# Kernel optimization log

Measured on AMD Instinct MI355X. Metric: run time of the kernel, lower is better.

## Reference

```python
import jax, jax.numpy as jnp
import numpy as np

M = 4  # mixture size of the AttentionStem value embedding

def unfold_windows(a, kh, kw, Hout, Wout):
    # a: [..., Hp, Wp] -> [..., Hout, Wout, kh, kw] (stride-1 sliding windows, cropped)
    rows = []
    for i in range(kh):
        cols = [a[..., i:i + Hout, j:j + Wout] for j in range(kw)]
        rows.append(jnp.stack(cols, axis=-1))
    return jnp.stack(rows, axis=-2)

def attention_stem(x, qw, kw_, vw, emb_a, emb_b, emb_mix, kh, kw, pad):
    # x: [B,Cin,H,W]; qw/kw_: [Cin,Co]; vw: [M,Cin,Co]; emb_a:[Co,kh]; emb_b:[Co,kw]; emb_mix:[M,Co]
    B, Cin, H, W = x.shape
    pl, pr, pt, pb = pad  # F.pad order (left,right,top,bottom)
    xp = jnp.pad(x, ((0, 0), (0, 0), (pt, pb), (pl, pr)))
    Hp, Wp = xp.shape[2], xp.shape[3]
    Hout = min(Hp - kh + 1, H)
    Wout = min(Wp - kw + 1, W)
    q = jnp.einsum('bchw,co->bohw', x[:, :, :Hout, :Wout], qw)       # 1x1 conv query
    k = jnp.einsum('bchw,co->bohw', xp, kw_)                          # 1x1 conv key on padded
    v = jnp.einsum('bchw,mco->mbohw', xp, vw)                         # m 1x1 conv values
    k_win = unfold_windows(k, kh, kw, Hout, Wout)                     # [B,Co,Ho,Wo,kh,kw]
    v_win = unfold_windows(v, kh, kw, Hout, Wout)                     # [M,B,Co,Ho,Wo,kh,kw]
    # mixture relative-position embedding, softmax over mixtures per (kh,kw) offset
    la = emb_mix @ emb_a                                              # [M,kh]
    lb = emb_mix @ emb_b                                              # [M,kw]
    emb = jax.nn.softmax(la[:, :, None] + lb[:, None, :], axis=0)     # [M,kh,kw]
    v_agg = jnp.einsum('mkl,mbohwkl->bohwkl', emb, v_win)             # [B,Co,Ho,Wo,kh,kw]
    K = kh * kw
    scores = jnp.einsum('bohw,bohwkl->bhwkl', q, k_win).reshape(B, Hout, Wout, K)
    attn = jax.nn.softmax(scores, axis=-1).reshape(B, Hout, Wout, kh, kw)
    out = jnp.einsum('bhwkl,bohwkl->bohw', attn, v_agg)               # [B,Co,Ho,Wo]
    return out

def bn_relu(x, g, b):
    # training-mode BatchNorm2d + ReLU
    mu = x.mean(axis=(0, 2, 3), keepdims=True)
    var = x.var(axis=(0, 2, 3), keepdims=True)
    y = (x - mu) * jax.lax.rsqrt(var + 1e-5) * g[None, :, None, None] + b[None, :, None, None]
    return jax.nn.relu(y)

def _params(key):
    ks = jax.random.split(key, 18)
    def w(k, shape):
        return jax.random.normal(k, shape, dtype=jnp.float32) * 0.1
    cfg = [(1, 64, 1, 5), (64, 128, 2, 5), (128, 16, 2, 5)]
    p = {}
    i = 0
    for s, (ci, co, kh, kw) in enumerate(cfg):
        p[f'p{s}_q'] = w(ks[i], (ci, co)); i += 1
        p[f'p{s}_k'] = w(ks[i], (ci, co)); i += 1
        p[f'p{s}_v'] = w(ks[i], (M, ci, co)); i += 1
        p[f'p{s}_ea'] = w(ks[i], (co, kh)); i += 1
        p[f'p{s}_eb'] = w(ks[i], (co, kw)); i += 1
        p[f'p{s}_em'] = w(ks[i], (M, co)); i += 1
        p[f'p{s}_g'] = jnp.ones((co,), jnp.float32)
        p[f'p{s}_b'] = jnp.zeros((co,), jnp.float32)
    return p

def setup_inputs() -> dict:
    key = jax.random.key(0)
    kx, kp = jax.random.split(key)
    inp = {'x': jax.random.normal(kx, (2, 1, 8, 3000), dtype=jnp.float32)}
    inp.update(_params(kp))
    return inp

def reference(x,
              p0_q, p0_k, p0_v, p0_ea, p0_eb, p0_em, p0_g, p0_b,
              p1_q, p1_k, p1_v, p1_ea, p1_eb, p1_em, p1_g, p1_b,
              p2_q, p2_k, p2_v, p2_ea, p2_eb, p2_em, p2_g, p2_b):
    h = attention_stem(x, p0_q, p0_k, p0_v, p0_ea, p0_eb, p0_em, 1, 5, (2, 2, 0, 0))
    h = bn_relu(h, p0_g, p0_b)[:, :, ::2, ::2]                        # MaxPool2d(1,2) == stride-2 subsample
    h = attention_stem(h, p1_q, p1_k, p1_v, p1_ea, p1_eb, p1_em, 2, 5, (2, 2, 1, 1))
    h = bn_relu(h, p1_g, p1_b)[:, :, ::2, ::2]
    h = attention_stem(h, p2_q, p2_k, p2_v, p2_ea, p2_eb, p2_em, 2, 5, (2, 2, 0, 0))
    h = bn_relu(h, p2_g, p2_b)
    B, C, H, W = h.shape
    nW = W // 56                                                       # AvgPool2d((1,56))
    return h[:, :, :, :nW * 56].reshape(B, C, H, nW, 56).mean(-1)
```

## Files before the change

kernel.cpp:

```cpp
#include <hip/hip_runtime.h>
#include <math.h>


#define TPB 256

__global__ void prep0_kernel(const float* __restrict__ ea,
                             const float* __restrict__ eb,
                             const float* __restrict__ em,
                             const float* __restrict__ qw,
                             const float* __restrict__ kw_,
                             const float* __restrict__ vw,
                             float* __restrict__ par) {
    const int M4 = 4, Co = 64, kw = 5;
    __shared__ float la[4];
    __shared__ float lb[20];
    __shared__ float embs[20];
    int tid = threadIdx.x;
    if (tid < 64) {
        float p = qw[tid] * kw_[tid];
#pragma unroll
        for (int d = 1; d < 64; d <<= 1) p += __shfl_xor(p, d, 64);
        if (tid == 0) par[0] = p;
    }
    if (tid >= 64 && tid < 64 + M4) {
        int m = tid - 64;
        float s = 0.f;
        for (int o = 0; o < Co; ++o) s += em[m * Co + o] * ea[o];
        la[m] = s;
    }
    if (tid >= 128 && tid < 128 + M4 * kw) {
        int r = tid - 128;
        int m = r / kw, l = r % kw;
        float s = 0.f;
        for (int o = 0; o < Co; ++o) s += em[m * Co + o] * eb[o * kw + l];
        lb[m * kw + l] = s;
    }
    __syncthreads();
    if (tid < 5) {
        float lg[4];
        float mx = -1e30f;
        for (int m = 0; m < M4; ++m) {
            lg[m] = la[m] + lb[m * kw + tid];
            mx = fmaxf(mx, lg[m]);
        }
        float sum = 0.f;
        for (int m = 0; m < M4; ++m) { lg[m] = expf(lg[m] - mx); sum += lg[m]; }
        float inv = 1.f / sum;
        for (int m = 0; m < M4; ++m) embs[tid * 4 + m] = lg[m] * inv;
    }
    __syncthreads();
    for (int e = tid; e < 5 * 64; e += blockDim.x) {
        int t = e / 64, o = e - t * 64;
        float s = 0.f;
        for (int m = 0; m < M4; ++m) s += embs[t * 4 + m] * vw[m * 64 + o];
        par[1 + e] = s;
    }
}

__global__ void attn_out0_kernel(const float* __restrict__ x,
                                 const float* __restrict__ par,
                                 float* __restrict__ h0raw,
                                 float2* __restrict__ part0) {
    __shared__ float wsh[5][256];
    __shared__ float vsh[5 * 64];
    __shared__ float wred[4][20];
    __shared__ float wfin[20];
    int tid = threadIdx.x;
    int b = blockIdx.y;
    int oz = blockIdx.z;
    int n0 = blockIdx.x * 256;
    int n = n0 + tid;
    for (int i = tid; i < 320; i += 256) vsh[i] = par[1 + i];
    float c0 = par[0];
    float warr[5];
    if (n < 24000) {
        int h = n / 3000, w = n - h * 3000;
        const float* xr = x + b * 24000 + h * 3000;
        float xc = xr[w];
        float xs[5], s[5];
#pragma unroll
        for (int t = 0; t < 5; ++t) {
            int col = w + t - 2;
            xs[t] = (col >= 0 && col < 3000) ? xr[col] : 0.f;
            s[t] = c0 * xc * xs[t];
        }
        float mx = s[0];
#pragma unroll
        for (int t = 1; t < 5; ++t) mx = fmaxf(mx, s[t]);
        float sum = 0.f;
#pragma unroll
        for (int t = 0; t < 5; ++t) { s[t] = expf(s[t] - mx); sum += s[t]; }
        float inv = 1.f / sum;
#pragma unroll
        for (int t = 0; t < 5; ++t) warr[t] = s[t] * inv * xs[t];
    } else {
#pragma unroll
        for (int t = 0; t < 5; ++t) warr[t] = 0.f;
    }
#pragma unroll
    for (int t = 0; t < 5; ++t) wsh[t][tid] = warr[t];
    float p[20];
#pragma unroll
    for (int t = 0; t < 5; ++t) p[t] = warr[t];
    {
        int k = 5;
#pragma unroll
        for (int t = 0; t < 5; ++t)
#pragma unroll
            for (int t2 = t; t2 < 5; ++t2) p[k++] = warr[t] * warr[t2];
    }
#pragma unroll
    for (int d = 1; d < 64; d <<= 1)
#pragma unroll
        for (int i = 0; i < 20; ++i) p[i] += __shfl_xor(p[i], d, 64);
    if ((tid & 63) == 0)
#pragma unroll
        for (int i = 0; i < 20; ++i) wred[tid >> 6][i] = p[i];
    __syncthreads();
    if (tid < 20)
        wfin[tid] = wred[0][tid] + wred[1][tid] + wred[2][tid] + wred[3][tid];
    __syncthreads();
    int jq = tid & 63, og = tid >> 6;
    int nq = n0 + jq * 4;
    int h = nq / 3000, w0 = nq - h * 3000;
    bool st = (nq < 24000) && ((h & 1) == 0);
    float wq[5][4];
#pragma unroll
    for (int t = 0; t < 5; ++t)
#pragma unroll
        for (int j = 0; j < 4; ++j) wq[t][j] = wsh[t][jq * 4 + j];
    int obase = oz * 32 + og * 8;
    for (int oi = 0; oi < 8; ++oi) {
        int o = obase + oi;
        float4 v = make_float4(0.f, 0.f, 0.f, 0.f);
#pragma unroll
        for (int t = 0; t < 5; ++t) {
            float vo = vsh[t * 64 + o];
            v.x = fmaf(wq[t][0], vo, v.x);
            v.y = fmaf(wq[t][1], vo, v.y);
            v.z = fmaf(wq[t][2], vo, v.z);
            v.w = fmaf(wq[t][3], vo, v.w);
        }
        if (st) {
            size_t base = ((size_t)b * 64 + o) * 6000 + (h >> 1) * 1500 + (w0 >> 1);
            *(float2*)&h0raw[base] = make_float2(v.x, v.z);
        }
    }
    if (tid < 32) {
        int o = oz * 32 + tid;
        float vt[5];
#pragma unroll
        for (int t = 0; t < 5; ++t) vt[t] = vsh[t * 64 + o];
        float s = 0.f, s2 = 0.f;
#pragma unroll
        for (int t = 0; t < 5; ++t) s = fmaf(vt[t], wfin[t], s);
        int k = 5;
#pragma unroll
        for (int t = 0; t < 5; ++t)
#pragma unroll
            for (int t2 = t; t2 < 5; ++t2) {
                float coef = (t == t2) ? vt[t] * vt[t] : 2.f * vt[t] * vt[t2];
                s2 = fmaf(coef, wfin[k], s2);
                ++k;
            }
        int chunk = b * gridDim.x + blockIdx.x;
        part0[(size_t)o * 188 + chunk] = make_float2(s, s2);
    }
}

__global__ void prep_stage1_kernel(const float* __restrict__ ea,
                                   const float* __restrict__ eb,
                                   const float* __restrict__ em,
                                   const float* __restrict__ qw,
                                   const float* __restrict__ kw_,
                                   const float* __restrict__ vw,
                                   float* __restrict__ G,
                                   float* __restrict__ Wy,
                                   float* __restrict__ embs1,
                                   const float2* __restrict__ part0,
                                   float* __restrict__ mr0) {
    const int M4 = 4, Co = 128, kh = 2, kw = 5;
    __shared__ float la[8];
    __shared__ float lb[20];
    __shared__ float embs[40];
    int tid = threadIdx.x;
    if (blockIdx.x == 0 && tid < 64) {
        double s = 0.0, s2 = 0.0;
        for (int i = 0; i < 188; ++i) {
            float2 p = part0[(size_t)tid * 188 + i];
            s += p.x; s2 += p.y;
        }
        double mean = s / 48000.0;
        double var = s2 / 48000.0 - mean * mean;
        mr0[tid] = (float)mean;
        mr0[64 + tid] = (float)(1.0 / sqrt(var + 1e-5));
    }
    if (tid < M4 * kh) {
        int m = tid / kh, k = tid % kh;
        float s = 0.f;
        for (int o = 0; o < Co; ++o) s += em[m * Co + o] * ea[o * kh + k];
        la[tid] = s;
    }
    if (tid >= 64 && tid < 64 + M4 * kw) {
        int r = tid - 64;
        int m = r / kw, l = r % kw;
        float s = 0.f;
        for (int o = 0; o < Co; ++o) s += em[m * Co + o] * eb[o * kw + l];
        lb[r] = s;
    }
    __syncthreads();
    if (tid < 10) {
        int k = tid / kw, l = tid % kw;
        float lg[4];
        float mx = -1e30f;
        for (int m = 0; m < M4; ++m) {
            lg[m] = la[m * kh + k] + lb[m * kw + l];
            mx = fmaxf(mx, lg[m]);
        }
        float sum = 0.f;
        for (int m = 0; m < M4; ++m) { lg[m] = expf(lg[m] - mx); sum += lg[m]; }
        float inv = 1.f / sum;
        for (int m = 0; m < M4; ++m) embs[tid * 4 + m] = lg[m] * inv;
    }
    __syncthreads();
    if (blockIdx.x == 0 && tid < 40) embs1[tid] = embs[tid];
    const int TOTG = 64 * 64;
    const int TOTW = 512 * 64;
    int nth = gridDim.x * blockDim.x;
    for (int e = blockIdx.x * blockDim.x + tid; e < TOTG + TOTW; e += nth) {
        if (e < TOTG) {
            int c = e >> 6, c2 = e & 63;
            float s = 0.f;
            for (int o = 0; o < 128; ++o)
                s = fmaf(qw[c * 128 + o], kw_[c2 * 128 + o], s);
            G[e] = s;
        } else {
            int e2 = e - TOTG;
            int r = e2 >> 6, c = e2 & 63;
            int m = r >> 7, o = r & 127;
            Wy[e2] = vw[(m * 64 + c) * 128 + o];
        }
    }
}

__global__ void prep_wcat_kernel(const float* __restrict__ ea,
                                 const float* __restrict__ eb,
                                 const float* __restrict__ em,
                                 const float* __restrict__ qw,
                                 const float* __restrict__ kw_,
                                 const float* __restrict__ vw,
                                 float* __restrict__ Wcat,
                                 int Co, int kh, int kw, int Cin,
                                 const float2* __restrict__ part,
                                 float* __restrict__ mr,
                                 int Cprev, int NCH, int count) {
    const int M4 = 4;
    __shared__ float la[8];
    __shared__ float lb[20];
    __shared__ float embs[40];
    int K = kh * kw;
    int tid = threadIdx.x;
    if (blockIdx.x == 0 && tid < Cprev) {
        double s = 0.0, s2 = 0.0;
        for (int i = 0; i < NCH; ++i) {
            float2 p = part[(size_t)tid * NCH + i];
            s += p.x; s2 += p.y;
        }
        double mean = s / count;
        double var = s2 / count - mean * mean;
        mr[tid] = (float)mean;
        mr[Cprev + tid] = (float)(1.0 / sqrt(var + 1e-5));
    }
    if (tid < M4 * kh) {
        int m = tid / kh, k = tid % kh;
        float s = 0.f;
        for (int o = 0; o < Co; ++o) s += em[m * Co + o] * ea[o * kh + k];
        la[tid] = s;
    }
    if (tid >= 64 && tid < 64 + M4 * kw) {
        int r = tid - 64;
        int m = r / kw, l = r % kw;
        float s = 0.f;
        for (int o = 0; o < Co; ++o) s += em[m * Co + o] * eb[o * kw + l];
        lb[r] = s;
    }
    __syncthreads();
    if (tid < K) {
        int k = tid / kw, l = tid % kw;
        float lg[4];
        float mx = -1e30f;
        for (int m = 0; m < M4; ++m) {
            lg[m] = la[m * kh + k] + lb[m * kw + l];
            mx = fmaxf(mx, lg[m]);
        }
        float sum = 0.f;
        for (int m = 0; m < M4; ++m) { lg[m] = expf(lg[m] - mx); sum += lg[m]; }
        float inv = 1.f / sum;
        for (int m = 0; m < M4; ++m) embs[tid * 4 + m] = lg[m] * inv;
    }
    __syncthreads();
    int Mtot = (2 + K) * Co;
    long long total = (long long)Mtot * Cin;
    for (long long e = (long long)blockIdx.x * blockDim.x + tid; e < total;
         e += (long long)gridDim.x * blockDim.x) {
        int m = (int)(e / Cin);
        int c = (int)(e - (long long)m * Cin);
        float val;
        if (m < Co) {
            val = qw[c * Co + m];
        } else if (m < 2 * Co) {
            val = kw_[c * Co + (m - Co)];
        } else {
            int mz = m - 2 * Co;
            int t = mz / Co;
            int o = mz - t * Co;
            val = 0.f;
            for (int mm = 0; mm < M4; ++mm)
                val += embs[t * 4 + mm] * vw[(mm * Cin + c) * Co + o];
        }
        Wcat[e] = val;
    }
}

__global__ void attn_v4_kernel(const float* __restrict__ G,
                               const float* __restrict__ xraw,
                               const float* __restrict__ mr,
                               const float* __restrict__ g,
                               const float* __restrict__ bb,
                               float* __restrict__ attn) {
    __shared__ float xw[64][2][68];
    __shared__ float gbuf[64][64];
    __shared__ float ssh[64][12];
    __shared__ float scb[64], sfb[64];
    int tid = threadIdx.x;
    int chunk = blockIdx.x;
    int ho = blockIdx.y;
    int b = blockIdx.z;
    int wo0 = chunk * 64;
    if (tid < 64) {
        float sc = mr[64 + tid] * g[tid];
        scb[tid] = sc;
        sfb[tid] = bb[tid] - mr[tid] * sc;
    }
    for (int e = tid; e < 4096; e += 256)
        gbuf[e >> 6][e & 63] = G[e];
    __syncthreads();
    for (int e = tid; e < 64 * 136; e += 256) {
        int c = e / 136;
        int r2 = e - c * 136;
        int r = r2 / 68, jj = r2 - r * 68;
        int row = ho - 1 + r;
        int col = wo0 + jj - 2;
        float v = 0.f;
        if (row >= 0 && col >= 0 && col < 1500) {
            float xv = xraw[((size_t)b * 64 + c) * 6000 + row * 1500 + col];
            v = fmaxf(fmaf(xv, scb[c], sfb[c]), 0.f);
        }
        xw[c][r][jj] = v;
    }
    __syncthreads();
    int j = tid & 63, cg = tid >> 6;
    float ul[16];
#pragma unroll
    for (int i = 0; i < 16; ++i) ul[i] = 0.f;
    for (int c = 0; c < 64; ++c) {
        float xv = xw[c][1][j + 2];
        float4 g0 = *(const float4*)&gbuf[c][cg * 16 + 0];
        float4 g1 = *(const float4*)&gbuf[c][cg * 16 + 4];
        float4 g2 = *(const float4*)&gbuf[c][cg * 16 + 8];
        float4 g3 = *(const float4*)&gbuf[c][cg * 16 + 12];
        ul[0]  = fmaf(g0.x, xv, ul[0]);  ul[1]  = fmaf(g0.y, xv, ul[1]);
        ul[2]  = fmaf(g0.z, xv, ul[2]);  ul[3]  = fmaf(g0.w, xv, ul[3]);
        ul[4]  = fmaf(g1.x, xv, ul[4]);  ul[5]  = fmaf(g1.y, xv, ul[5]);
        ul[6]  = fmaf(g1.z, xv, ul[6]);  ul[7]  = fmaf(g1.w, xv, ul[7]);
        ul[8]  = fmaf(g2.x, xv, ul[8]);  ul[9]  = fmaf(g2.y, xv, ul[9]);
        ul[10] = fmaf(g2.z, xv, ul[10]); ul[11] = fmaf(g2.w, xv, ul[11]);
        ul[12] = fmaf(g3.x, xv, ul[12]); ul[13] = fmaf(g3.y, xv, ul[13]);
        ul[14] = fmaf(g3.z, xv, ul[14]); ul[15] = fmaf(g3.w, xv, ul[15]);
    }
    __syncthreads();
#pragma unroll
    for (int i = 0; i < 16; ++i) gbuf[cg * 16 + i][j] = ul[i];
    __syncthreads();
    int t0 = cg, t1 = cg + 4, t2 = cg + 8;
    int dk0 = t0 / 5, dl0 = t0 % 5;
    int dk1 = t1 / 5, dl1 = t1 % 5;
    int dk2 = (t2 < 10) ? 1 : 0, dl2 = (t2 < 10) ? (t2 - 5) : 0;
    float s0 = 0.f, s1 = 0.f, s2v = 0.f;
    for (int c = 0; c < 64; ++c) {
        float uv = gbuf[c][j];
        s0 = fmaf(uv, xw[c][dk0][j + dl0], s0);
        s1 = fmaf(uv, xw[c][dk1][j + dl1], s1);
        if (t2 < 10) s2v = fmaf(uv, xw[c][dk2][j + dl2], s2v);
    }
    ssh[j][t0] = s0;
    ssh[j][t1] = s1;
    if (t2 < 10) ssh[j][t2] = s2v;
    __syncthreads();
    if (tid < 64 && wo0 + tid < 1500) {
        float sc[10];
        float mx = -1e30f;
#pragma unroll
        for (int t = 0; t < 10; ++t) { sc[t] = ssh[tid][t]; mx = fmaxf(mx, sc[t]); }
        float sum = 0.f;
#pragma unroll
        for (int t = 0; t < 10; ++t) { sc[t] = expf(sc[t] - mx); sum += sc[t]; }
        float inv = 1.f / sum;
        int n = ho * 1500 + wo0 + tid;
#pragma unroll
        for (int t = 0; t < 10; ++t)
            attn[((size_t)b * 10 + t) * 6000 + n] = sc[t] * inv;
    }
}

__launch_bounds__(256, 4)
__global__ void gemm_qkbn_kernel(const float* __restrict__ A,
                                 const float* __restrict__ xraw,
                                 const float* __restrict__ mr,
                                 const float* __restrict__ g,
                                 const float* __restrict__ bb,
                                 float* __restrict__ qk,
                                 float* __restrict__ z,
                                 int M, int N, int K, int twoCo) {
    __shared__ float As[32][132];
    __shared__ float Bs[32][132];
    __shared__ float scale[128], shift[128];
    int tid = threadIdx.x;
    int b = blockIdx.z;
    int m0 = blockIdx.y * 128, n0 = blockIdx.x * 128;
    int Mz = M - twoCo;
    float acc[8][8] = {{0.f}};
    int am = tid >> 1, ak = (tid & 1) * 16;
    int bk = tid >> 3, bn = (tid & 7) * 16;
    int tm = tid & 15, tn = tid >> 4;
    for (int c = tid; c < K; c += 256) {
        float sc = mr[K + c] * g[c];
        scale[c] = sc;
        shift[c] = bb[c] - mr[c] * sc;
    }
    __syncthreads();
    for (int k0 = 0; k0 < K; k0 += 32) {
        {
            int mA = m0 + am;
            const float* Ap = A + (size_t)mA * K + k0 + ak;
#pragma unroll
            for (int q = 0; q < 4; ++q) {
                float4 v = (mA < M) ? *(const float4*)(Ap + q * 4)
                                    : make_float4(0.f, 0.f, 0.f, 0.f);
                int kk = ak + q * 4;
                As[kk + 0][am] = v.x;
                As[kk + 1][am] = v.y;
                As[kk + 2][am] = v.z;
                As[kk + 3][am] = v.w;
            }
        }
        {
            int c = k0 + bk;
            float sc = scale[c], sf = shift[c];
            const float* Xp = xraw + ((size_t)b * K + c) * N + n0 + bn;
            if (n0 + 128 <= N) {
#pragma unroll
                for (int q = 0; q < 4; ++q) {
                    float4 v = *(const float4*)(Xp + q * 4);
                    v.x = fmaxf(fmaf(v.x, sc, sf), 0.f);
                    v.y = fmaxf(fmaf(v.y, sc, sf), 0.f);
                    v.z = fmaxf(fmaf(v.z, sc, sf), 0.f);
                    v.w = fmaxf(fmaf(v.w, sc, sf), 0.f);
                    *(float4*)&Bs[bk][bn + q * 4] = v;
                }
            } else {
#pragma unroll
                for (int q = 0; q < 16; ++q) {
                    int n = n0 + bn + q;
                    Bs[bk][bn + q] = (n < N) ? fmaxf(fmaf(Xp[q], sc, sf), 0.f) : 0.f;
                }
            }
        }
        __syncthreads();
#pragma unroll 8
        for (int k = 0; k < 32; ++k) {
            float4 a0 = *(const float4*)&As[k][tm * 4];
            float4 a1 = *(const float4*)&As[k][64 + tm * 4];
            float4 b0 = *(const float4*)&Bs[k][tn * 4];
            float4 b1 = *(const float4*)&Bs[k][64 + tn * 4];
            float av[8] = {a0.x, a0.y, a0.z, a0.w, a1.x, a1.y, a1.z, a1.w};
            float bv[8] = {b0.x, b0.y, b0.z, b0.w, b1.x, b1.y, b1.z, b1.w};
#pragma unroll
            for (int i = 0; i < 8; ++i)
#pragma unroll
                for (int j = 0; j < 8; ++j)
                    acc[i][j] = fmaf(av[i], bv[j], acc[i][j]);
        }
        __syncthreads();
    }
    bool fullN = (n0 + 128 <= N);
#pragma unroll
    for (int iq = 0; iq < 2; ++iq) {
        int mb = m0 + iq * 64 + tm * 4;
        if (mb >= M) continue;
        if (mb < twoCo) {
#pragma unroll
            for (int jq = 0; jq < 2; ++jq)
#pragma unroll
                for (int jj = 0; jj < 4; ++jj) {
                    int n = n0 + jq * 64 + tn * 4 + jj;
                    if (n < N) {
                        float4 v = make_float4(acc[iq * 4 + 0][jq * 4 + jj],
                                               acc[iq * 4 + 1][jq * 4 + jj],
                                               acc[iq * 4 + 2][jq * 4 + jj],
                                               acc[iq * 4 + 3][jq * 4 + jj]);
                        *(float4*)&qk[((size_t)b * N + n) * twoCo + mb] = v;
                    }
                }
        } else {
#pragma unroll
            for (int i = 0; i < 4; ++i) {
                int row = mb + i - twoCo;
                float* zp = &z[((size_t)b * Mz + row) * N];
#pragma unroll
                for (int jq = 0; jq < 2; ++jq) {
                    int nb_ = n0 + jq * 64 + tn * 4;
                    if (fullN) {
                        *(float4*)&zp[nb_] = make_float4(acc[iq * 4 + i][jq * 4 + 0],
                                                         acc[iq * 4 + i][jq * 4 + 1],
                                                         acc[iq * 4 + i][jq * 4 + 2],
                                                         acc[iq * 4 + i][jq * 4 + 3]);
                    } else {
#pragma unroll
                        for (int jj = 0; jj < 4; ++jj)
                            if (nb_ + jj < N) zp[nb_ + jj] = acc[iq * 4 + i][jq * 4 + jj];
                    }
                }
            }
        }
    }
}

__global__ void combine1_kernel(const float* __restrict__ y,
                                const float* __restrict__ attn,
                                const float* __restrict__ embs1,
                                float* __restrict__ h1raw,
                                float2* __restrict__ part1) {
    __shared__ float yw[4][2][256];
    __shared__ float embl[40];
    __shared__ float sh[TPB], sh2[TPB];
    int tid = threadIdx.x;
    int bx = blockIdx.x;
    int ho = bx / 6, wc = bx - ho * 6;
    int wo0 = wc * 250;
    int by = blockIdx.y;
    int b = by >> 7, o = by & 127;
    if (tid < 40) embl[tid] = embs1[tid];
    for (int e = tid; e < 4 * 2 * 256; e += 256) {
        int m = e >> 9;
        int rem = e & 511;
        int r = rem >> 8, j = rem & 255;
        int row = ho - 1 + r;
        int col = wo0 - 2 + j;
        float v = 0.f;
        if (j < 254 && row >= 0 && row < 4 && col >= 0 && col < 1500)
            v = y[((size_t)b * 512 + m * 128 + o) * 6000 + row * 1500 + col];
        yw[m][r][j] = v;
    }
    __syncthreads();
    float val = 0.f;
    int wo = wo0 + tid;
    if (tid < 250) {
        int n = ho * 1500 + wo;
        float a[10];
#pragma unroll
        for (int t = 0; t < 10; ++t)
            a[t] = attn[((size_t)b * 10 + t) * 6000 + n];
#pragma unroll
        for (int m = 0; m < 4; ++m) {
#pragma unroll
            for (int dk = 0; dk < 2; ++dk)
#pragma unroll
                for (int dl = 0; dl < 5; ++dl) {
                    int t = dk * 5 + dl;
                    val = fmaf(a[t] * embl[t * 4 + m], yw[m][dk][tid + dl], val);
                }
        }
        if (((ho | wo) & 1) == 0)
            h1raw[((size_t)b * 128 + o) * 1500 + (ho >> 1) * 750 + (wo >> 1)] = val;
    }
    sh[tid] = (tid < 250) ? val : 0.f;
    sh2[tid] = (tid < 250) ? val * val : 0.f;
    __syncthreads();
    for (int st = TPB / 2; st > 0; st >>= 1) {
        if (tid < st) { sh[tid] += sh[tid + st]; sh2[tid] += sh2[tid + st]; }
        __syncthreads();
    }
    if (tid == 0) {
        int chunk = b * 24 + bx;
        part1[(size_t)o * 48 + chunk] = make_float2(sh[0], sh2[0]);
    }
}

template <int KH, int KW, int CO, int NPB>
__global__ void attn_v3_kernel(const float* __restrict__ qk,
                               float* __restrict__ attn,
                               int H, int W, int Ho, int Wo, int pt, int pl) {
    const int K = KH * KW;
    __shared__ float ssh[NPB][K];
    int tid = threadIdx.x;
    int b = blockIdx.y;
    int ln = tid / K, t = tid - ln * K;
    int Nout = Ho * Wo;
    int n = blockIdx.x * NPB + ln;
    bool active = (tid < NPB * K) && (n < Nout);
    int HWin = H * W;
    float sv = 0.f;
    if (active) {
        int ho = n / Wo, wo = n - ho * Wo;
        int row = ho + t / KW - pt, col = wo + t % KW - pl;
        if (row >= 0 && row < H && col >= 0 && col < W) {
            const float* qp = qk + ((size_t)b * HWin + ho * W + wo) * (2 * CO);
            const float* kp = qk + ((size_t)b * HWin + (size_t)row * W + col) * (2 * CO) + CO;
#pragma unroll
            for (int o = 0; o < CO; o += 4) {
                float4 q4 = *(const float4*)(qp + o);
                float4 k4 = *(const float4*)(kp + o);
                sv += q4.x * k4.x + q4.y * k4.y + q4.z * k4.z + q4.w * k4.w;
            }
        }
        ssh[ln][t] = sv;
    }
    __syncthreads();
    if (active) {
        float mx = ssh[ln][0];
#pragma unroll
        for (int tt = 1; tt < K; ++tt) mx = fmaxf(mx, ssh[ln][tt]);
        float sum = 0.f;
#pragma unroll
        for (int tt = 0; tt < K; ++tt) sum += expf(ssh[ln][tt] - mx);
        float num = expf(sv - mx);
        attn[((size_t)b * K + t) * Nout + n] = num / sum;
    }
}

template <int KH, int KW>
__global__ void combine_stats_kernel(const float* __restrict__ z,
                                     const float* __restrict__ attn,
                                     float* __restrict__ out,
                                     float2* __restrict__ part,
                                     int Co, int Mz,
                                     int H, int W, int Ho, int Wo,
                                     int pt, int pl) {
    const int K = KH * KW;
    int tid = threadIdx.x;
    int bc = blockIdx.y;
    int b = bc / Co, o = bc - b * Co;
    int Nout = Ho * Wo, Nin = H * W;
    int n = blockIdx.x * blockDim.x + tid;
    float val = 0.f;
    if (n < Nout) {
        int ho = n / Wo, wo = n - ho * Wo;
#pragma unroll
        for (int dk = 0; dk < KH; ++dk) {
            int row = ho + dk - pt;
            if (row < 0 || row >= H) continue;
#pragma unroll
            for (int dl = 0; dl < KW; ++dl) {
                int col = wo + dl - pl;
                if (col < 0 || col >= W) continue;
                int t = dk * KW + dl;
                float a = attn[((size_t)b * K + t) * Nout + n];
                float zv = z[((size_t)b * Mz + t * Co + o) * Nin + row * W + col];
                val = fmaf(a, zv, val);
            }
        }
        out[((size_t)b * Co + o) * Nout + n] = val;
    }
    __shared__ float sh[TPB], sh2[TPB];
    sh[tid] = (n < Nout) ? val : 0.f;
    sh2[tid] = (n < Nout) ? val * val : 0.f;
    __syncthreads();
    for (int st = TPB / 2; st > 0; st >>= 1) {
        if (tid < st) { sh[tid] += sh[tid + st]; sh2[tid] += sh2[tid + st]; }
        __syncthreads();
    }
    if (tid == 0) {
        int chunk = b * gridDim.x + blockIdx.x;
        part[(size_t)o * (2 * gridDim.x) + chunk] = make_float2(sh[0], sh2[0]);
    }
}

__global__ void bn_avg_final_kernel(const float* __restrict__ x,
                                    const float2* __restrict__ part,
                                    const float* __restrict__ g,
                                    const float* __restrict__ bb,
                                    float* __restrict__ out,
                                    int B, int C, int W, int nW, int NCH) {
    int idx = blockIdx.x * blockDim.x + threadIdx.x;
    int N = B * C * nW;
    if (idx >= N) return;
    int j = idx % nW; int r = idx / nW;
    int c = r % C; int b = r / C;
    double s = 0.0, s2 = 0.0;
    for (int i = 0; i < NCH; ++i) {
        float2 p = part[(size_t)c * NCH + i];
        s += p.x; s2 += p.y;
    }
    double cnt = (double)B * W;
    double mean = s / cnt;
    double var = s2 / cnt - mean * mean;
    float rstd = (float)(1.0 / sqrt(var + 1e-5));
    float meanf = (float)mean, gg = g[c], bo = bb[c];
    const float* xb = x + ((long long)b * C + c) * W + j * 56;
    float acc = 0.f;
    for (int i = 0; i < 56; ++i) {
        float yn = (xb[i] - meanf) * rstd * gg + bo;
        acc += fmaxf(yn, 0.f);
    }
    out[idx] = acc * (1.f / 56.f);
}

extern "C" void kernel_launch(void* const* d_in, const int* in_sizes, int n_in,
                              void* d_out, int out_size, void* d_ws, size_t ws_size,
                              hipStream_t stream) {
    const float* x   = (const float*)d_in[0];
    const float* qw0 = (const float*)d_in[1];
    const float* kw0 = (const float*)d_in[2];
    const float* vw0 = (const float*)d_in[3];
    const float* ea0 = (const float*)d_in[4];
    const float* eb0 = (const float*)d_in[5];
    const float* em0 = (const float*)d_in[6];
    const float* g0  = (const float*)d_in[7];
    const float* b0  = (const float*)d_in[8];
    const float* qw1 = (const float*)d_in[9];
    const float* kw1 = (const float*)d_in[10];
    const float* vw1 = (const float*)d_in[11];
    const float* ea1 = (const float*)d_in[12];
    const float* eb1 = (const float*)d_in[13];
    const float* em1 = (const float*)d_in[14];
    const float* g1  = (const float*)d_in[15];
    const float* b1  = (const float*)d_in[16];
    const float* qw2 = (const float*)d_in[17];
    const float* kw2 = (const float*)d_in[18];
    const float* vw2 = (const float*)d_in[19];
    const float* ea2 = (const float*)d_in[20];
    const float* eb2 = (const float*)d_in[21];
    const float* em2 = (const float*)d_in[22];
    const float* g2  = (const float*)d_in[23];
    const float* b2  = (const float*)d_in[24];
    float* outp = (float*)d_out;
    (void)ws_size; (void)in_sizes; (void)n_in; (void)out_size;

    float* ws = (float*)d_ws;
    size_t off = 0;
    auto alloc = [&](size_t n) { float* p = ws + off; off += (n + 63) & ~(size_t)63; return p; };

    float* par0   = alloc(321);
    float* part0  = alloc(64 * 188 * 2);
    float* mr0    = alloc(128);
    float* h0raw  = alloc(2 * 64 * 6000);
    float* G1     = alloc(64 * 64);
    float* Wy1    = alloc(512 * 64);
    float* embs1  = alloc(40);
    float* attn1  = alloc(2 * 10 * 6000);
    float* ybuf   = alloc(2 * 512 * 6000);
    float* part1  = alloc(128 * 48 * 2);
    float* mr1    = alloc(256);
    float* h1raw  = alloc(2 * 128 * 1500);
    float* Wcat2  = alloc(192 * 128);
    float* qk2    = alloc(2 * 1500 * 32);
    float* z2     = alloc(2 * 160 * 1500);
    float* attn2  = alloc(2 * 10 * 750);
    float* part2  = alloc(16 * 6 * 2);
    float* s2     = alloc(2 * 16 * 750);

    auto grid = [](int n) { return (n + TPB - 1) / TPB; };

    prep0_kernel<<<1, TPB, 0, stream>>>(ea0, eb0, em0, qw0, kw0, vw0, par0);
    {
        dim3 g(94, 2, 2);
        attn_out0_kernel<<<g, TPB, 0, stream>>>(x, par0, h0raw, (float2*)part0);
    }
    prep_stage1_kernel<<<64, TPB, 0, stream>>>(ea1, eb1, em1, qw1, kw1, vw1,
        G1, Wy1, embs1, (const float2*)part0, mr0);
    {
        dim3 g(24, 4, 2);
        attn_v4_kernel<<<g, TPB, 0, stream>>>(G1, h0raw, mr0, g0, b0, attn1);
    }
    {
        dim3 g(47, 4, 2);
        gemm_qkbn_kernel<<<g, TPB, 0, stream>>>(Wy1, h0raw, mr0, g0, b0,
            ybuf , ybuf, 512, 6000, 64, 0);
    }
    {
        dim3 g(24, 256);
        combine1_kernel<<<g, TPB, 0, stream>>>(ybuf, attn1, embs1,
            h1raw, (float2*)part1);
    }
    prep_wcat_kernel<<<24, TPB, 0, stream>>>(ea2, eb2, em2, qw2, kw2, vw2, Wcat2,
        16, 2, 5, 128, (const float2*)part1, mr1, 128, 48, 12000);
    {
        dim3 g(12, 2, 2);
        gemm_qkbn_kernel<<<g, TPB, 0, stream>>>(Wcat2, h1raw, mr1, g1, b1,
            qk2, z2, 192, 1500, 128, 32);
    }
    {
        dim3 g(750 / 25, 2);
        attn_v3_kernel<2, 5, 16, 25><<<g, TPB, 0, stream>>>(qk2, attn2,
            2, 750, 1, 750, 0, 2);
    }
    {
        dim3 g(3, 2 * 16);
        combine_stats_kernel<2, 5><<<g, TPB, 0, stream>>>(z2, attn2, s2,
            (float2*)part2, 16, 160, 2, 750, 1, 750, 0, 2);
    }
    bn_avg_final_kernel<<<grid(2 * 16 * 13), TPB, 0, stream>>>(s2, (const float2*)part2,
        g2, b2, outp, 2, 16, 750, 13, 6);
}
```

Baseline: 259.9 us.

## Fuse prep kernels and stage kernels to cut launch count

Folds all three stages' parameter-prep work into extra blocks of the stage-0 attention kernel, and merges the stage-1 attention and value GEMM into one dual-role kernel. BN statistics reduction moves into consumers. Stage-2 attention scoring is fused with the combine and stats step, and a specialized stage-2 GEMM replaces the generic one. This removes roughly five kernel launches and intermediate buffers, at the cost of redundant per-block prep work and larger, more heterogeneous kernels.

```diff
diff --git a/kernel.cpp b/kernel.cpp
--- a/kernel.cpp
+++ b/kernel.cpp
@@ -4,74 +4,176 @@
 
 #define TPB 256
 
-__global__ void prep0_kernel(const float* __restrict__ ea,
-                             const float* __restrict__ eb,
-                             const float* __restrict__ em,
-                             const float* __restrict__ qw,
-                             const float* __restrict__ kw_,
-                             const float* __restrict__ vw,
-                             float* __restrict__ par) {
-    const int M4 = 4, Co = 64, kw = 5;
-    __shared__ float la[4];
-    __shared__ float lb[20];
-    __shared__ float embs[20];
+__global__ void stage0_kernel(const float* __restrict__ x,
+                              const float* __restrict__ qw0, const float* __restrict__ kw0,
+                              const float* __restrict__ vw0, const float* __restrict__ ea0,
+                              const float* __restrict__ eb0, const float* __restrict__ em0,
+                              const float* __restrict__ qw1, const float* __restrict__ kw1,
+                              const float* __restrict__ vw1, const float* __restrict__ ea1,
+                              const float* __restrict__ eb1, const float* __restrict__ em1,
+                              const float* __restrict__ qw2, const float* __restrict__ kw2,
+                              const float* __restrict__ vw2, const float* __restrict__ ea2,
+                              const float* __restrict__ eb2, const float* __restrict__ em2,
+                              float* __restrict__ h0raw,
+                              float2* __restrict__ part0,
+                              float* __restrict__ G,
+                              float* __restrict__ Wy,
+                              float* __restrict__ embs1g,
+                              float* __restrict__ Wcat2) {
     int tid = threadIdx.x;
+    int bx = blockIdx.x;
+    if (bx >= 94) {
+        if (blockIdx.y != 0 || blockIdx.z != 0) return;
+        int role = bx - 94;
+        __shared__ float la[8], lb[20], embs[40];
+        if (role == 0) {
+            if (tid < 8) {
+                int m = tid / 2, k = tid % 2;
+                float s = 0.f;
+                for (int o = 0; o < 128; ++o) s += em1[m * 128 + o] * ea1[o * 2 + k];
+                la[tid] = s;
+            }
+            if (tid >= 64 && tid < 84) {
+                int r = tid - 64;
+                int m = r / 5, l = r % 5;
+                float s = 0.f;
+                for (int o = 0; o < 128; ++o) s += em1[m * 128 + o] * eb1[o * 5 + l];
+                lb[r] = s;
+            }
+            __syncthreads();
+            if (tid < 10) {
+                int k = tid / 5, l = tid % 5;
+                float lg[4], mx = -1e30f;
+                for (int m = 0; m < 4; ++m) {
+                    lg[m] = la[m * 2 + k] + lb[m * 5 + l];
+                    mx = fmaxf(mx, lg[m]);
+                }
+                float sum = 0.f;
+                for (int m = 0; m < 4; ++m) { lg[m] = expf(lg[m] - mx); sum += lg[m]; }
+                float inv = 1.f / sum;
+                for (int m = 0; m < 4; ++m) embs[tid * 4 + m] = lg[m] * inv;
+            }
+            __syncthreads();
+            if (tid < 40) embs1g[tid] = embs[tid];
+            for (int e = tid; e < 2048; e += 256) {
+                int c = e >> 6, c2 = e & 63;
+                float s = 0.f;
+                for (int o = 0; o < 128; ++o)
+                    s = fmaf(qw1[c * 128 + o], kw1[c2 * 128 + o], s);
+                G[e] = s;
+            }
+        } else if (role == 1) {
+            for (int e = 2048 + tid; e < 4096; e += 256) {
+                int c = e >> 6, c2 = e & 63;
+                float s = 0.f;
+                for (int o = 0; o < 128; ++o)
+                    s = fmaf(qw1[c * 128 + o], kw1[c2 * 128 + o], s);
+                G[e] = s;
+            }
+        } else if (role == 2 || role == 3) {
+            int base = (role - 2) * 16384;
+            for (int e = base + tid; e < base + 16384; e += 256) {
+                int r = e >> 6, c = e & 63;
+                int m = r >> 7, o = r & 127;
+                Wy[e] = vw1[(m * 64 + c) * 128 + o];
+            }
+        } else {
+            if (tid < 8) {
+                int m = tid / 2, k = tid % 2;
+                float s = 0.f;
+                for (int o = 0; o < 16; ++o) s += em2[m * 16 + o] * ea2[o * 2 + k];
+                la[tid] = s;
+            }
+            if (tid >= 64 && tid < 84) {
+                int r = tid - 64;
+                int m = r / 5, l = r % 5;
+                float s = 0.f;
+                for (int o = 0; o < 16; ++o) s += em2[m * 16 + o] * eb2[o * 5 + l];
+                lb[r] = s;
+            }
+            __syncthreads();
+            if (tid < 10) {
+                int k = tid / 5, l = tid % 5;
+                float lg[4], mx = -1e30f;
+                for (int m = 0; m < 4; ++m) {
+                    lg[m] = la[m * 2 + k] + lb[m * 5 + l];
+                    mx = fmaxf(mx, lg[m]);
+                }
+                float sum = 0.f;
+                for (int m = 0; m < 4; ++m) { lg[m] = expf(lg[m] - mx); sum += lg[m]; }
+                float inv = 1.f / sum;
+                for (int m = 0; m < 4; ++m) embs[tid * 4 + m] = lg[m] * inv;
+            }
+            __syncthreads();
+            int base = (role - 4) * 6144;
+            for (int e = base + tid; e < base + 6144; e += 256) {
+                int row = e >> 7, c = e & 127;
+                float val;
+                if (row < 16) {
+                    val = qw2[c * 16 + row];
+                } else if (row < 32) {
+                    val = kw2[c * 16 + (row - 16)];
+                } else {
+                    int t = (row - 32) >> 4, o = (row - 32) & 15;
+                    val = 0.f;
+                    for (int m = 0; m < 4; ++m)
+                        val += embs[t * 4 + m] * vw2[(m * 128 + c) * 16 + o];
+                }
+                Wcat2[e] = val;
+            }
+        }
+        return;
+    }
+    __shared__ float wsh[5][256];
+    __shared__ float vsh[320];
+    __shared__ float wred[4][20];
+    __shared__ float wfin[20];
+    __shared__ float la0[4], lb0[20], embs0[20];
+    __shared__ float c0s;
+    int b = blockIdx.y;
+    int oz = blockIdx.z;
+    int n0 = bx * 256;
+    int n = n0 + tid;
     if (tid < 64) {
-        float p = qw[tid] * kw_[tid];
+        float p = qw0[tid] * kw0[tid];
 #pragma unroll
         for (int d = 1; d < 64; d <<= 1) p += __shfl_xor(p, d, 64);
-        if (tid == 0) par[0] = p;
-    }
-    if (tid >= 64 && tid < 64 + M4) {
+        if (tid == 0) c0s = p;
+    }
+    if (tid >= 64 && tid < 68) {
         int m = tid - 64;
         float s = 0.f;
-        for (int o = 0; o < Co; ++o) s += em[m * Co + o] * ea[o];
-        la[m] = s;
-    }
-    if (tid >= 128 && tid < 128 + M4 * kw) {
+        for (int o = 0; o < 64; ++o) s += em0[m * 64 + o] * ea0[o];
+        la0[m] = s;
+    }
+    if (tid >= 128 && tid < 148) {
         int r = tid - 128;
-        int m = r / kw, l = r % kw;
+        int m = r / 5, l = r % 5;
         float s = 0.f;
-        for (int o = 0; o < Co; ++o) s += em[m * Co + o] * eb[o * kw + l];
-        lb[m * kw + l] = s;
+        for (int o = 0; o < 64; ++o) s += em0[m * 64 + o] * eb0[o * 5 + l];
+        lb0[m * 5 + l] = s;
     }
     __syncthreads();
     if (tid < 5) {
-        float lg[4];
-        float mx = -1e30f;
-        for (int m = 0; m < M4; ++m) {
-            lg[m] = la[m] + lb[m * kw + tid];
+        float lg[4], mx = -1e30f;
+        for (int m = 0; m < 4; ++m) {
+            lg[m] = la0[m] + lb0[m * 5 + tid];
             mx = fmaxf(mx, lg[m]);
         }
         float sum = 0.f;
-        for (int m = 0; m < M4; ++m) { lg[m] = expf(lg[m] - mx); sum += lg[m]; }
+        for (int m = 0; m < 4; ++m) { lg[m] = expf(lg[m] - mx); sum += lg[m]; }
         float inv = 1.f / sum;
-        for (int m = 0; m < M4; ++m) embs[tid * 4 + m] = lg[m] * inv;
+        for (int m = 0; m < 4; ++m) embs0[tid * 4 + m] = lg[m] * inv;
     }
     __syncthreads();
-    for (int e = tid; e < 5 * 64; e += blockDim.x) {
+    for (int e = tid; e < 320; e += 256) {
         int t = e / 64, o = e - t * 64;
         float s = 0.f;
-        for (int m = 0; m < M4; ++m) s += embs[t * 4 + m] * vw[m * 64 + o];
-        par[1 + e] = s;
-    }
-}
-
-__global__ void attn_out0_kernel(const float* __restrict__ x,
-                                 const float* __restrict__ par,
-                                 float* __restrict__ h0raw,
-                                 float2* __restrict__ part0) {
-    __shared__ float wsh[5][256];
-    __shared__ float vsh[5 * 64];
-    __shared__ float wred[4][20];
-    __shared__ float wfin[20];
-    int tid = threadIdx.x;
-    int b = blockIdx.y;
-    int oz = blockIdx.z;
-    int n0 = blockIdx.x * 256;
-    int n = n0 + tid;
-    for (int i = tid; i < 320; i += 256) vsh[i] = par[1 + i];
-    float c0 = par[0];
+        for (int m = 0; m < 4; ++m) s += embs0[t * 4 + m] * vw0[m * 64 + o];
+        vsh[e] = s;
+    }
+    __syncthreads();
+    float c0 = c0s;
     float warr[5];
     if (n < 24000) {
         int h = n / 3000, w = n - h * 3000;
@@ -163,360 +265,199 @@
                 s2 = fmaf(coef, wfin[k], s2);
                 ++k;
             }
-        int chunk = b * gridDim.x + blockIdx.x;
+        int chunk = b * 94 + bx;
         part0[(size_t)o * 188 + chunk] = make_float2(s, s2);
     }
 }
 
-__global__ void prep_stage1_kernel(const float* __restrict__ ea,
-                                   const float* __restrict__ eb,
-                                   const float* __restrict__ em,
-                                   const float* __restrict__ qw,
-                                   const float* __restrict__ kw_,
-                                   const float* __restrict__ vw,
-                                   float* __restrict__ G,
-                                   float* __restrict__ Wy,
-                                   float* __restrict__ embs1,
+__launch_bounds__(256)
+__global__ void stage1_dual_kernel(const float* __restrict__ G,
+                                   const float* __restrict__ Wy,
+                                   const float* __restrict__ xraw,
                                    const float2* __restrict__ part0,
-                                   float* __restrict__ mr0) {
-    const int M4 = 4, Co = 128, kh = 2, kw = 5;
-    __shared__ float la[8];
-    __shared__ float lb[20];
-    __shared__ float embs[40];
+                                   const float* __restrict__ g0,
+                                   const float* __restrict__ b0,
+                                   float* __restrict__ attn,
+                                   float* __restrict__ ybuf) {
+    __shared__ float smem[13696];
     int tid = threadIdx.x;
-    if (blockIdx.x == 0 && tid < 64) {
-        double s = 0.0, s2 = 0.0;
-        for (int i = 0; i < 188; ++i) {
-            float2 p = part0[(size_t)tid * 188 + i];
-            s += p.x; s2 += p.y;
-        }
-        double mean = s / 48000.0;
-        double var = s2 / 48000.0 - mean * mean;
-        mr0[tid] = (float)mean;
-        mr0[64 + tid] = (float)(1.0 / sqrt(var + 1e-5));
-    }
-    if (tid < M4 * kh) {
-        int m = tid / kh, k = tid % kh;
-        float s = 0.f;
-        for (int o = 0; o < Co; ++o) s += em[m * Co + o] * ea[o * kh + k];
-        la[tid] = s;
-    }
-    if (tid >= 64 && tid < 64 + M4 * kw) {
-        int r = tid - 64;
-        int m = r / kw, l = r % kw;
-        float s = 0.f;
-        for (int o = 0; o < Co; ++o) s += em[m * Co + o] * eb[o * kw + l];
-        lb[r] = s;
-    }
-    __syncthreads();
-    if (tid < 10) {
-        int k = tid / kw, l = tid % kw;
-        float lg[4];
-        float mx = -1e30f;
-        for (int m = 0; m < M4; ++m) {
-            lg[m] = la[m * kh + k] + lb[m * kw + l];
-            mx = fmaxf(mx, lg[m]);
-        }
-        float sum = 0.f;
-        for (int m = 0; m < M4; ++m) { lg[m] = expf(lg[m] - mx); sum += lg[m]; }
-        float inv = 1.f / sum;
-        for (int m = 0; m < M4; ++m) embs[tid * 4 + m] = lg[m] * inv;
-    }
-    __syncthreads();
-    if (blockIdx.x == 0 && tid < 40) embs1[tid] = embs[tid];
-    const int TOTG = 64 * 64;
-    const int TOTW = 512 * 64;
-    int nth = gridDim.x * blockDim.x;
-    for (int e = blockIdx.x * blockDim.x + tid; e < TOTG + TOTW; e += nth) {
-        if (e < TOTG) {
-            int c = e >> 6, c2 = e & 63;
-            float s = 0.f;
-            for (int o = 0; o < 128; ++o)
-                s = fmaf(qw[c * 128 + o], kw_[c2 * 128 + o], s);
-            G[e] = s;
-        } else {
-            int e2 = e - TOTG;
-            int r = e2 >> 6, c = e2 & 63;
-            int m = r >> 7, o = r & 127;
-            Wy[e2] = vw[(m * 64 + c) * 128 + o];
-        }
-    }
-}
-
-__global__ void prep_wcat_kernel(const float* __restrict__ ea,
-                                 const float* __restrict__ eb,
-                                 const float* __restrict__ em,
-                                 const float* __restrict__ qw,
-                                 const float* __restrict__ kw_,
-                                 const float* __restrict__ vw,
-                                 float* __restrict__ Wcat,
-                                 int Co, int kh, int kw, int Cin,
-                                 const float2* __restrict__ part,
-                                 float* __restrict__ mr,
-                                 int Cprev, int NCH, int count) {
-    const int M4 = 4;
-    __shared__ float la[8];
-    __shared__ float lb[20];
-    __shared__ float embs[40];
-    int K = kh * kw;
-    int tid = threadIdx.x;
-    if (blockIdx.x == 0 && tid < Cprev) {
-        double s = 0.0, s2 = 0.0;
-        for (int i = 0; i < NCH; ++i) {
-            float2 p = part[(size_t)tid * NCH + i];
-            s += p.x; s2 += p.y;
-        }
-        double mean = s / count;
-        double var = s2 / count - mean * mean;
-        mr[tid] = (float)mean;
-        mr[Cprev + tid] = (float)(1.0 / sqrt(var + 1e-5));
-    }
-    if (tid < M4 * kh) {
-        int m = tid / kh, k = tid % kh;
-        float s = 0.f;
-        for (int o = 0; o < Co; ++o) s += em[m * Co + o] * ea[o * kh + k];
-        la[tid] = s;
-    }
-    if (tid >= 64 && tid < 64 + M4 * kw) {
-        int r = tid - 64;
-        int m = r / kw, l = r % kw;
-        float s = 0.f;
-        for (int o = 0; o < Co; ++o) s += em[m * Co + o] * eb[o * kw + l];
-        lb[r] = s;
-    }
-    __syncthreads();
-    if (tid < K) {
-        int k = tid / kw, l = tid % kw;
-        float lg[4];
-        float mx = -1e30f;
-        for (int m = 0; m < M4; ++m) {
-            lg[m] = la[m * kh + k] + lb[m * kw + l];
-            mx = fmaxf(mx, lg[m]);
-        }
-        float sum = 0.f;
-        for (int m = 0; m < M4; ++m) { lg[m] = expf(lg[m] - mx); sum += lg[m]; }
-        float inv = 1.f / sum;
-        for (int m = 0; m < M4; ++m) embs[tid * 4 + m] = lg[m] * inv;
-    }
-    __syncthreads();
-    int Mtot = (2 + K) * Co;
-    long long total = (long long)Mtot * Cin;
-    for (long long e = (long long)blockIdx.x * blockDim.x + tid; e < total;
-         e += (long long)gridDim.x * blockDim.x) {
-        int m = (int)(e / Cin);
-        int c = (int)(e - (long long)m * Cin);
-        float val;
-        if (m < Co) {
-            val = qw[c * Co + m];
-        } else if (m < 2 * Co) {
-            val = kw_[c * Co + (m - Co)];
-        } else {
-            int mz = m - 2 * Co;
-            int t = mz / Co;
-            int o = mz - t * Co;
-            val = 0.f;
-            for (int mm = 0; mm < M4; ++mm)
-                val += embs[t * 4 + mm] * vw[(mm * Cin + c) * Co + o];
-        }
-        Wcat[e] = val;
-    }
-}
-
-__global__ void attn_v4_kernel(const float* __restrict__ G,
-                               const float* __restrict__ xraw,
-                               const float* __restrict__ mr,
-                               const float* __restrict__ g,
-                               const float* __restrict__ bb,
-                               float* __restrict__ attn) {
-    __shared__ float xw[64][2][68];
-    __shared__ float gbuf[64][64];
-    __shared__ float ssh[64][12];
-    __shared__ float scb[64], sfb[64];
-    int tid = threadIdx.x;
-    int chunk = blockIdx.x;
-    int ho = blockIdx.y;
-    int b = blockIdx.z;
-    int wo0 = chunk * 64;
-    if (tid < 64) {
-        float sc = mr[64 + tid] * g[tid];
-        scb[tid] = sc;
-        sfb[tid] = bb[tid] - mr[tid] * sc;
-    }
-    for (int e = tid; e < 4096; e += 256)
-        gbuf[e >> 6][e & 63] = G[e];
-    __syncthreads();
-    for (int e = tid; e < 64 * 136; e += 256) {
-        int c = e / 136;
-        int r2 = e - c * 136;
-        int r = r2 / 68, jj = r2 - r * 68;
-        int row = ho - 1 + r;
-        int col = wo0 + jj - 2;
-        float v = 0.f;
-        if (row >= 0 && col >= 0 && col < 1500) {
-            float xv = xraw[((size_t)b * 64 + c) * 6000 + row * 1500 + col];
-            v = fmaxf(fmaf(xv, scb[c], sfb[c]), 0.f);
-        }
-        xw[c][r][jj] = v;
-    }
-    __syncthreads();
-    int j = tid & 63, cg = tid >> 6;
-    float ul[16];
-#pragma unroll
-    for (int i = 0; i < 16; ++i) ul[i] = 0.f;
-    for (int c = 0; c < 64; ++c) {
-        float xv = xw[c][1][j + 2];
-        float4 g0 = *(const float4*)&gbuf[c][cg * 16 + 0];
-        float4 g1 = *(const float4*)&gbuf[c][cg * 16 + 4];
-        float4 g2 = *(const float4*)&gbuf[c][cg * 16 + 8];
-        float4 g3 = *(const float4*)&gbuf[c][cg * 16 + 12];
-        ul[0]  = fmaf(g0.x, xv, ul[0]);  ul[1]  = fmaf(g0.y, xv, ul[1]);
-        ul[2]  = fmaf(g0.z, xv, ul[2]);  ul[3]  = fmaf(g0.w, xv, ul[3]);
-        ul[4]  = fmaf(g1.x, xv, ul[4]);  ul[5]  = fmaf(g1.y, xv, ul[5]);
-        ul[6]  = fmaf(g1.z, xv, ul[6]);  ul[7]  = fmaf(g1.w, xv, ul[7]);
-        ul[8]  = fmaf(g2.x, xv, ul[8]);  ul[9]  = fmaf(g2.y, xv, ul[9]);
-        ul[10] = fmaf(g2.z, xv, ul[10]); ul[11] = fmaf(g2.w, xv, ul[11]);
-        ul[12] = fmaf(g3.x, xv, ul[12]); ul[13] = fmaf(g3.y, xv, ul[13]);
-        ul[14] = fmaf(g3.z, xv, ul[14]); ul[15] = fmaf(g3.w, xv, ul[15]);
-    }
-    __syncthreads();
-#pragma unroll
-    for (int i = 0; i < 16; ++i) gbuf[cg * 16 + i][j] = ul[i];
-    __syncthreads();
-    int t0 = cg, t1 = cg + 4, t2 = cg + 8;
-    int dk0 = t0 / 5, dl0 = t0 % 5;
-    int dk1 = t1 / 5, dl1 = t1 % 5;
-    int dk2 = (t2 < 10) ? 1 : 0, dl2 = (t2 < 10) ? (t2 - 5) : 0;
-    float s0 = 0.f, s1 = 0.f, s2v = 0.f;
-    for (int c = 0; c < 64; ++c) {
-        float uv = gbuf[c][j];
-        s0 = fmaf(uv, xw[c][dk0][j + dl0], s0);
-        s1 = fmaf(uv, xw[c][dk1][j + dl1], s1);
-        if (t2 < 10) s2v = fmaf(uv, xw[c][dk2][j + dl2], s2v);
-    }
-    ssh[j][t0] = s0;
-    ssh[j][t1] = s1;
-    if (t2 < 10) ssh[j][t2] = s2v;
-    __syncthreads();
-    if (tid < 64 && wo0 + tid < 1500) {
-        float sc[10];
-        float mx = -1e30f;
-#pragma unroll
-        for (int t = 0; t < 10; ++t) { sc[t] = ssh[tid][t]; mx = fmaxf(mx, sc[t]); }
-        float sum = 0.f;
-#pragma unroll
-        for (int t = 0; t < 10; ++t) { sc[t] = expf(sc[t] - mx); sum += sc[t]; }
-        float inv = 1.f / sum;
-        int n = ho * 1500 + wo0 + tid;
-#pragma unroll
-        for (int t = 0; t < 10; ++t)
-            attn[((size_t)b * 10 + t) * 6000 + n] = sc[t] * inv;
-    }
-}
-
-__launch_bounds__(256, 4)
-__global__ void gemm_qkbn_kernel(const float* __restrict__ A,
-                                 const float* __restrict__ xraw,
-                                 const float* __restrict__ mr,
-                                 const float* __restrict__ g,
-                                 const float* __restrict__ bb,
-                                 float* __restrict__ qk,
-                                 float* __restrict__ z,
-                                 int M, int N, int K, int twoCo) {
-    __shared__ float As[32][132];
-    __shared__ float Bs[32][132];
-    __shared__ float scale[128], shift[128];
-    int tid = threadIdx.x;
-    int b = blockIdx.z;
-    int m0 = blockIdx.y * 128, n0 = blockIdx.x * 128;
-    int Mz = M - twoCo;
-    float acc[8][8] = {{0.f}};
-    int am = tid >> 1, ak = (tid & 1) * 16;
-    int bk = tid >> 3, bn = (tid & 7) * 16;
-    int tm = tid & 15, tn = tid >> 4;
-    for (int c = tid; c < K; c += 256) {
-        float sc = mr[K + c] * g[c];
-        scale[c] = sc;
-        shift[c] = bb[c] - mr[c] * sc;
-    }
-    __syncthreads();
-    for (int k0 = 0; k0 < K; k0 += 32) {
-        {
-            int mA = m0 + am;
-            const float* Ap = A + (size_t)mA * K + k0 + ak;
-#pragma unroll
-            for (int q = 0; q < 4; ++q) {
-                float4 v = (mA < M) ? *(const float4*)(Ap + q * 4)
-                                    : make_float4(0.f, 0.f, 0.f, 0.f);
-                int kk = ak + q * 4;
-                As[kk + 0][am] = v.x;
-                As[kk + 1][am] = v.y;
-                As[kk + 2][am] = v.z;
-                As[kk + 3][am] = v.w;
-            }
-        }
-        {
-            int c = k0 + bk;
-            float sc = scale[c], sf = shift[c];
-            const float* Xp = xraw + ((size_t)b * K + c) * N + n0 + bn;
-            if (n0 + 128 <= N) {
+    int bx = blockIdx.x;
+    if (bx < 192) {
+        float (*xw)[2][68] = (float(*)[2][68])smem;
+        float (*gbuf)[64]  = (float(*)[64])(smem + 8704);
+        float (*ssh)[12]   = (float(*)[12])(smem + 12800);
+        float* scb = smem + 13568;
+        float* sfb = smem + 13632;
+        int b = bx / 96;
+        int rem = bx % 96;
+        int ho = rem / 24, chunk = rem % 24;
+        int wo0 = chunk * 64;
+        if (tid < 64) {
+            double s = 0.0, s2 = 0.0;
+            const float2* pp = part0 + (size_t)tid * 188;
+            for (int i = 0; i < 188; ++i) { float2 p = pp[i]; s += p.x; s2 += p.y; }
+            double mean = s / 48000.0;
+            double var = s2 / 48000.0 - mean * mean;
+            float rstd = (float)(1.0 / sqrt(var + 1e-5));
+            float sc = rstd * g0[tid];
+            scb[tid] = sc;
+            sfb[tid] = b0[tid] - (float)mean * sc;
+        }
+        for (int e = tid; e < 4096; e += 256)
+            gbuf[e >> 6][e & 63] = G[e];
+        __syncthreads();
+        for (int e = tid; e < 64 * 136; e += 256) {
+            int c = e / 136;
+            int r2 = e - c * 136;
+            int r = r2 / 68, jj = r2 - r * 68;
+            int row = ho - 1 + r;
+            int col = wo0 + jj - 2;
+            float v = 0.f;
+            if (row >= 0 && col >= 0 && col < 1500) {
+                float xv = xraw[((size_t)b * 64 + c) * 6000 + row * 1500 + col];
+                v = fmaxf(fmaf(xv, scb[c], sfb[c]), 0.f);
+            }
+            xw[c][r][jj] = v;
+        }
+        __syncthreads();
+        int j = tid & 63, cg = tid >> 6;
+        float ul[16];
+#pragma unroll
+        for (int i = 0; i < 16; ++i) ul[i] = 0.f;
+        for (int c = 0; c < 64; ++c) {
+            float xv = xw[c][1][j + 2];
+            float4 q0 = *(const float4*)&gbuf[c][cg * 16 + 0];
+            float4 q1 = *(const float4*)&gbuf[c][cg * 16 + 4];
+            float4 q2 = *(const float4*)&gbuf[c][cg * 16 + 8];
+            float4 q3 = *(const float4*)&gbuf[c][cg * 16 + 12];
+            ul[0]  = fmaf(q0.x, xv, ul[0]);  ul[1]  = fmaf(q0.y, xv, ul[1]);
+            ul[2]  = fmaf(q0.z, xv, ul[2]);  ul[3]  = fmaf(q0.w, xv, ul[3]);
+            ul[4]  = fmaf(q1.x, xv, ul[4]);  ul[5]  = fmaf(q1.y, xv, ul[5]);
+            ul[6]  = fmaf(q1.z, xv, ul[6]);  ul[7]  = fmaf(q1.w, xv, ul[7]);
+            ul[8]  = fmaf(q2.x, xv, ul[8]);  ul[9]  = fmaf(q2.y, xv, ul[9]);
+            ul[10] = fmaf(q2.z, xv, ul[10]); ul[11] = fmaf(q2.w, xv, ul[11]);
+            ul[12] = fmaf(q3.x, xv, ul[12]); ul[13] = fmaf(q3.y, xv, ul[13]);
+            ul[14] = fmaf(q3.z, xv, ul[14]); ul[15] = fmaf(q3.w, xv, ul[15]);
+        }
+        __syncthreads();
+#pragma unroll
+        for (int i = 0; i < 16; ++i) gbuf[cg * 16 + i][j] = ul[i];
+        __syncthreads();
+        int t0 = cg, t1 = cg + 4, t2 = cg + 8;
+        int dk0 = t0 / 5, dl0 = t0 % 5;
+        int dk1 = t1 / 5, dl1 = t1 % 5;
+        int dk2 = (t2 < 10) ? 1 : 0, dl2 = (t2 < 10) ? (t2 - 5) : 0;
+        float s0 = 0.f, s1 = 0.f, s2v = 0.f;
+        for (int c = 0; c < 64; ++c) {
+            float uv = gbuf[c][j];
+            s0 = fmaf(uv, xw[c][dk0][j + dl0], s0);
+            s1 = fmaf(uv, xw[c][dk1][j + dl1], s1);
+            if (t2 < 10) s2v = fmaf(uv, xw[c][dk2][j + dl2], s2v);
+        }
+        ssh[j][t0] = s0;
+        ssh[j][t1] = s1;
+        if (t2 < 10) ssh[j][t2] = s2v;
+        __syncthreads();
+        if (tid < 64 && wo0 + tid < 1500) {
+            float sc[10];
+            float mx = -1e30f;
+#pragma unroll
+            for (int t = 0; t < 10; ++t) { sc[t] = ssh[tid][t]; mx = fmaxf(mx, sc[t]); }
+            float sum = 0.f;
+#pragma unroll
+            for (int t = 0; t < 10; ++t) { sc[t] = expf(sc[t] - mx); sum += sc[t]; }
+            float inv = 1.f / sum;
+            int n = ho * 1500 + wo0 + tid;
+#pragma unroll
+            for (int t = 0; t < 10; ++t)
+                attn[((size_t)b * 10 + t) * 6000 + n] = sc[t] * inv;
+        }
+    } else {
+        float (*As)[132] = (float(*)[132])smem;
+        float (*Bs)[132] = (float(*)[132])(smem + 4224);
+        float* scale = smem + 8448;
+        float* shift = smem + 8512;
+        int r = bx - 192;
+        int b = r / 188;
+        int rem = r % 188;
+        int mt = rem / 47, nt = rem % 47;
+        int m0 = mt * 128, n0 = nt * 128;
+        if (tid < 64) {
+            double s = 0.0, s2 = 0.0;
+            const float2* pp = part0 + (size_t)tid * 188;
+            for (int i = 0; i < 188; ++i) { float2 p = pp[i]; s += p.x; s2 += p.y; }
+            double mean = s / 48000.0;
+            double var = s2 / 48000.0 - mean * mean;
+            float rstd = (float)(1.0 / sqrt(var + 1e-5));
+            float sc = rstd * g0[tid];
+            scale[tid] = sc;
+            shift[tid] = b0[tid] - (float)mean * sc;
+        }
+        __syncthreads();
+        float acc[8][8] = {{0.f}};
+        int am = tid >> 1, ak = (tid & 1) * 16;
+        int bk = tid >> 3, bn = (tid & 7) * 16;
+        int tm = tid & 15, tn = tid >> 4;
+        for (int k0 = 0; k0 < 64; k0 += 32) {
+            {
+                const float* Ap = Wy + (size_t)(m0 + am) * 64 + k0 + ak;
 #pragma unroll
                 for (int q = 0; q < 4; ++q) {
-                    float4 v = *(const float4*)(Xp + q * 4);
-                    v.x = fmaxf(fmaf(v.x, sc, sf), 0.f);
-                    v.y = fmaxf(fmaf(v.y, sc, sf), 0.f);
-                    v.z = fmaxf(fmaf(v.z, sc, sf), 0.f);
-                    v.w = fmaxf(fmaf(v.w, sc, sf), 0.f);
-                    *(float4*)&Bs[bk][bn + q * 4] = v;
-                }
-            } else {
-#pragma unroll
-                for (int q = 0; q < 16; ++q) {
-                    int n = n0 + bn + q;
-                    Bs[bk][bn + q] = (n < N) ? fmaxf(fmaf(Xp[q], sc, sf), 0.f) : 0.f;
-                }
-            }
-        }
-        __syncthreads();
+                    float4 v = *(const float4*)(Ap + q * 4);
+                    int kk = ak + q * 4;
+                    As[kk + 0][am] = v.x;
+                    As[kk + 1][am] = v.y;
+                    As[kk + 2][am] = v.z;
+                    As[kk + 3][am] = v.w;
+                }
+            }
+            {
+                int c = k0 + bk;
+                float sc = scale[c], sf = shift[c];
+                const float* Xp = xraw + ((size_t)b * 64 + c) * 6000 + n0 + bn;
+                if (n0 + 128 <= 6000) {
+#pragma unroll
+                    for (int q = 0; q < 4; ++q) {
+                        float4 v = *(const float4*)(Xp + q * 4);
+                        v.x = fmaxf(fmaf(v.x, sc, sf), 0.f);
+                        v.y = fmaxf(fmaf(v.y, sc, sf), 0.f);
+                        v.z = fmaxf(fmaf(v.z, sc, sf), 0.f);
+                        v.w = fmaxf(fmaf(v.w, sc, sf), 0.f);
+                        *(float4*)&Bs[bk][bn + q * 4] = v;
+                    }
+                } else {
+#pragma unroll
+                    for (int q = 0; q < 16; ++q) {
+                        int n = n0 + bn + q;
+                        Bs[bk][bn + q] = (n < 6000) ? fmaxf(fmaf(Xp[q], sc, sf), 0.f) : 0.f;
+                    }
+                }
+            }
+            __syncthreads();
 #pragma unroll 8
-        for (int k = 0; k < 32; ++k) {
-            float4 a0 = *(const float4*)&As[k][tm * 4];
-            float4 a1 = *(const float4*)&As[k][64 + tm * 4];
-            float4 b0 = *(const float4*)&Bs[k][tn * 4];
-            float4 b1 = *(const float4*)&Bs[k][64 + tn * 4];
-            float av[8] = {a0.x, a0.y, a0.z, a0.w, a1.x, a1.y, a1.z, a1.w};
-            float bv[8] = {b0.x, b0.y, b0.z, b0.w, b1.x, b1.y, b1.z, b1.w};
-#pragma unroll
-            for (int i = 0; i < 8; ++i)
-#pragma unroll
-                for (int j = 0; j < 8; ++j)
-                    acc[i][j] = fmaf(av[i], bv[j], acc[i][j]);
-        }
-        __syncthreads();
-    }
-    bool fullN = (n0 + 128 <= N);
-#pragma unroll
-    for (int iq = 0; iq < 2; ++iq) {
-        int mb = m0 + iq * 64 + tm * 4;
-        if (mb >= M) continue;
-        if (mb < twoCo) {
-#pragma unroll
-            for (int jq = 0; jq < 2; ++jq)
-#pragma unroll
-                for (int jj = 0; jj < 4; ++jj) {
-                    int n = n0 + jq * 64 + tn * 4 + jj;
-                    if (n < N) {
-                        float4 v = make_float4(acc[iq * 4 + 0][jq * 4 + jj],
-                                               acc[iq * 4 + 1][jq * 4 + jj],
-                                               acc[iq * 4 + 2][jq * 4 + jj],
-                                               acc[iq * 4 + 3][jq * 4 + jj]);
-                        *(float4*)&qk[((size_t)b * N + n) * twoCo + mb] = v;
-                    }
-                }
-        } else {
+            for (int k = 0; k < 32; ++k) {
+                float4 a0 = *(const float4*)&As[k][tm * 4];
+                float4 a1 = *(const float4*)&As[k][64 + tm * 4];
+                float4 bb0 = *(const float4*)&Bs[k][tn * 4];
+                float4 bb1 = *(const float4*)&Bs[k][64 + tn * 4];
+                float av[8] = {a0.x, a0.y, a0.z, a0.w, a1.x, a1.y, a1.z, a1.w};
+                float bv[8] = {bb0.x, bb0.y, bb0.z, bb0.w, bb1.x, bb1.y, bb1.z, bb1.w};
+#pragma unroll
+                for (int i = 0; i < 8; ++i)
+#pragma unroll
+                    for (int jx = 0; jx < 8; ++jx)
+                        acc[i][jx] = fmaf(av[i], bv[jx], acc[i][jx]);
+            }
+            __syncthreads();
+        }
+        bool fullN = (n0 + 128 <= 6000);
+#pragma unroll
+        for (int iq = 0; iq < 2; ++iq) {
+            int mb = m0 + iq * 64 + tm * 4;
 #pragma unroll
             for (int i = 0; i < 4; ++i) {
-                int row = mb + i - twoCo;
-                float* zp = &z[((size_t)b * Mz + row) * N];
+                int row = mb + i;
+                float* zp = &ybuf[((size_t)b * 512 + row) * 6000];
 #pragma unroll
                 for (int jq = 0; jq < 2; ++jq) {
                     int nb_ = n0 + jq * 64 + tn * 4;
@@ -528,7 +469,7 @@
                     } else {
 #pragma unroll
                         for (int jj = 0; jj < 4; ++jj)
-                            if (nb_ + jj < N) zp[nb_ + jj] = acc[iq * 4 + i][jq * 4 + jj];
+                            if (nb_ + jj < 6000) zp[nb_ + jj] = acc[iq * 4 + i][jq * 4 + jj];
                     }
                 }
             }
@@ -597,93 +538,200 @@
     }
 }
 
-template <int KH, int KW, int CO, int NPB>
-__global__ void attn_v3_kernel(const float* __restrict__ qk,
-                               float* __restrict__ attn,
-                               int H, int W, int Ho, int Wo, int pt, int pl) {
-    const int K = KH * KW;
-    __shared__ float ssh[NPB][K];
+__launch_bounds__(256, 4)
+__global__ void gemm2_kernel(const float* __restrict__ A,
+                             const float* __restrict__ xraw,
+                             const float2* __restrict__ part1,
+                             const float* __restrict__ g1,
+                             const float* __restrict__ b1,
+                             float* __restrict__ qk,
+                             float* __restrict__ z) {
+    const int M = 192, N = 1500, K = 128, twoCo = 32, Mz = 160;
+    __shared__ float As[32][132];
+    __shared__ float Bs[32][132];
+    __shared__ float scale[128], shift[128];
     int tid = threadIdx.x;
-    int b = blockIdx.y;
-    int ln = tid / K, t = tid - ln * K;
-    int Nout = Ho * Wo;
-    int n = blockIdx.x * NPB + ln;
-    bool active = (tid < NPB * K) && (n < Nout);
-    int HWin = H * W;
-    float sv = 0.f;
-    if (active) {
-        int ho = n / Wo, wo = n - ho * Wo;
-        int row = ho + t / KW - pt, col = wo + t % KW - pl;
-        if (row >= 0 && row < H && col >= 0 && col < W) {
-            const float* qp = qk + ((size_t)b * HWin + ho * W + wo) * (2 * CO);
-            const float* kp = qk + ((size_t)b * HWin + (size_t)row * W + col) * (2 * CO) + CO;
-#pragma unroll
-            for (int o = 0; o < CO; o += 4) {
-                float4 q4 = *(const float4*)(qp + o);
-                float4 k4 = *(const float4*)(kp + o);
-                sv += q4.x * k4.x + q4.y * k4.y + q4.z * k4.z + q4.w * k4.w;
-            }
-        }
-        ssh[ln][t] = sv;
+    int b = blockIdx.z;
+    int m0 = blockIdx.y * 128, n0 = blockIdx.x * 128;
+    float acc[8][8] = {{0.f}};
+    int am = tid >> 1, ak = (tid & 1) * 16;
+    int bk = tid >> 3, bn = (tid & 7) * 16;
+    int tm = tid & 15, tn = tid >> 4;
+    if (tid < 128) {
+        double s = 0.0, s2 = 0.0;
+        const float2* pp = part1 + (size_t)tid * 48;
+        for (int i = 0; i < 48; ++i) { float2 p = pp[i]; s += p.x; s2 += p.y; }
+        double mean = s / 12000.0;
+        double var = s2 / 12000.0 - mean * mean;
+        float rstd = (float)(1.0 / sqrt(var + 1e-5));
+        float sc = rstd * g1[tid];
+        scale[tid] = sc;
+        shift[tid] = b1[tid] - (float)mean * sc;
     }
     __syncthreads();
-    if (active) {
-        float mx = ssh[ln][0];
-#pragma unroll
-        for (int tt = 1; tt < K; ++tt) mx = fmaxf(mx, ssh[ln][tt]);
+    for (int k0 = 0; k0 < K; k0 += 32) {
+        {
+            int mA = m0 + am;
+            const float* Ap = A + (size_t)mA * K + k0 + ak;
+#pragma unroll
+            for (int q = 0; q < 4; ++q) {
+                float4 v = (mA < M) ? *(const float4*)(Ap + q * 4)
+                                    : make_float4(0.f, 0.f, 0.f, 0.f);
+                int kk = ak + q * 4;
+                As[kk + 0][am] = v.x;
+                As[kk + 1][am] = v.y;
+                As[kk + 2][am] = v.z;
+                As[kk + 3][am] = v.w;
+            }
+        }
+        {
+            int c = k0 + bk;
+            float sc = scale[c], sf = shift[c];
+            const float* Xp = xraw + ((size_t)b * K + c) * N + n0 + bn;
+            if (n0 + 128 <= N) {
+#pragma unroll
+                for (int q = 0; q < 4; ++q) {
+                    float4 v = *(const float4*)(Xp + q * 4);
+                    v.x = fmaxf(fmaf(v.x, sc, sf), 0.f);
+                    v.y = fmaxf(fmaf(v.y, sc, sf), 0.f);
+                    v.z = fmaxf(fmaf(v.z, sc, sf), 0.f);
+                    v.w = fmaxf(fmaf(v.w, sc, sf), 0.f);
+                    *(float4*)&Bs[bk][bn + q * 4] = v;
+                }
+            } else {
+#pragma unroll
+                for (int q = 0; q < 16; ++q) {
+                    int n = n0 + bn + q;
+                    Bs[bk][bn + q] = (n < N) ? fmaxf(fmaf(Xp[q], sc, sf), 0.f) : 0.f;
+                }
+            }
+        }
+        __syncthreads();
+#pragma unroll 8
+        for (int k = 0; k < 32; ++k) {
+            float4 a0 = *(const float4*)&As[k][tm * 4];
+            float4 a1 = *(const float4*)&As[k][64 + tm * 4];
+            float4 bb0 = *(const float4*)&Bs[k][tn * 4];
+            float4 bb1 = *(const float4*)&Bs[k][64 + tn * 4];
+            float av[8] = {a0.x, a0.y, a0.z, a0.w, a1.x, a1.y, a1.z, a1.w};
+            float bv[8] = {bb0.x, bb0.y, bb0.z, bb0.w, bb1.x, bb1.y, bb1.z, bb1.w};
+#pragma unroll
+            for (int i = 0; i < 8; ++i)
+#pragma unroll
+                for (int jx = 0; jx < 8; ++jx)
+                    acc[i][jx] = fmaf(av[i], bv[jx], acc[i][jx]);
+        }
+        __syncthreads();
+    }
+    bool fullN = (n0 + 128 <= N);
+#pragma unroll
+    for (int iq = 0; iq < 2; ++iq) {
+        int mb = m0 + iq * 64 + tm * 4;
+        if (mb >= M) continue;
+        if (mb < twoCo) {
+#pragma unroll
+            for (int jq = 0; jq < 2; ++jq)
+#pragma unroll
+                for (int jj = 0; jj < 4; ++jj) {
+                    int n = n0 + jq * 64 + tn * 4 + jj;
+                    if (n < N) {
+                        float4 v = make_float4(acc[iq * 4 + 0][jq * 4 + jj],
+                                               acc[iq * 4 + 1][jq * 4 + jj],
+                                               acc[iq * 4 + 2][jq * 4 + jj],
+                                               acc[iq * 4 + 3][jq * 4 + jj]);
+                        *(float4*)&qk[((size_t)b * N + n) * twoCo + mb] = v;
+                    }
+                }
+        } else {
+#pragma unroll
+            for (int i = 0; i < 4; ++i) {
+                int row = mb + i - twoCo;
+                float* zp = &z[((size_t)b * Mz + row) * N];
+#pragma unroll
+                for (int jq = 0; jq < 2; ++jq) {
+                    int nb_ = n0 + jq * 64 + tn * 4;
+                    if (fullN) {
+                        *(float4*)&zp[nb_] = make_float4(acc[iq * 4 + i][jq * 4 + 0],
+                                                         acc[iq * 4 + i][jq * 4 + 1],
+                                                         acc[iq * 4 + i][jq * 4 + 2],
+                                                         acc[iq * 4 + i][jq * 4 + 3]);
+                    } else {
+#pragma unroll
+                        for (int jj = 0; jj < 4; ++jj)
+                            if (nb_ + jj < N) zp[nb_ + jj] = acc[iq * 4 + i][jq * 4 + jj];
+                    }
+                }
+            }
+        }
+    }
+}
+
+__global__ void attn_combine2_kernel(const float* __restrict__ qk,
+                                     const float* __restrict__ z,
+                                     float* __restrict__ out,
+                                     float2* __restrict__ part) {
+    __shared__ float sh[TPB], sh2[TPB];
+    int tid = threadIdx.x;
+    int bx = blockIdx.x;
+    int by = blockIdx.y;
+    int b = by >> 4, o = by & 15;
+    int n = bx * 256 + tid;
+    float val = 0.f;
+    if (n < 750) {
+        const float* qp = qk + ((size_t)b * 1500 + n) * 32;
+        float q[16];
+#pragma unroll
+        for (int i = 0; i < 16; i += 4) {
+            float4 v = *(const float4*)(qp + i);
+            q[i] = v.x; q[i + 1] = v.y; q[i + 2] = v.z; q[i + 3] = v.w;
+        }
+        float s[10];
+        bool valid[10];
+        int col[10];
+#pragma unroll
+        for (int dk = 0; dk < 2; ++dk)
+#pragma unroll
+            for (int dl = 0; dl < 5; ++dl) {
+                int t = dk * 5 + dl;
+                int c = n + dl - 2;
+                valid[t] = (c >= 0 && c < 750);
+                col[t] = dk * 750 + c;
+                float sv = 0.f;
+                if (valid[t]) {
+                    const float* kp = qk + ((size_t)b * 1500 + col[t]) * 32 + 16;
+#pragma unroll
+                    for (int i = 0; i < 16; i += 4) {
+                        float4 k4 = *(const float4*)(kp + i);
+                        sv += q[i] * k4.x + q[i + 1] * k4.y + q[i + 2] * k4.z + q[i + 3] * k4.w;
+                    }
+                }
+                s[t] = sv;
+            }
+        float mx = s[0];
+#pragma unroll
+        for (int t = 1; t < 10; ++t) mx = fmaxf(mx, s[t]);
         float sum = 0.f;
 #pragma unroll
-        for (int tt = 0; tt < K; ++tt) sum += expf(ssh[ln][tt] - mx);
-        float num = expf(sv - mx);
-        attn[((size_t)b * K + t) * Nout + n] = num / sum;
-    }
-}
-
-template <int KH, int KW>
-__global__ void combine_stats_kernel(const float* __restrict__ z,
-                                     const float* __restrict__ attn,
-                                     float* __restrict__ out,
-                                     float2* __restrict__ part,
-                                     int Co, int Mz,
-                                     int H, int W, int Ho, int Wo,
-                                     int pt, int pl) {
-    const int K = KH * KW;
-    int tid = threadIdx.x;
-    int bc = blockIdx.y;
-    int b = bc / Co, o = bc - b * Co;
-    int Nout = Ho * Wo, Nin = H * W;
-    int n = blockIdx.x * blockDim.x + tid;
-    float val = 0.f;
-    if (n < Nout) {
-        int ho = n / Wo, wo = n - ho * Wo;
-#pragma unroll
-        for (int dk = 0; dk < KH; ++dk) {
-            int row = ho + dk - pt;
-            if (row < 0 || row >= H) continue;
-#pragma unroll
-            for (int dl = 0; dl < KW; ++dl) {
-                int col = wo + dl - pl;
-                if (col < 0 || col >= W) continue;
-                int t = dk * KW + dl;
-                float a = attn[((size_t)b * K + t) * Nout + n];
-                float zv = z[((size_t)b * Mz + t * Co + o) * Nin + row * W + col];
-                val = fmaf(a, zv, val);
-            }
-        }
-        out[((size_t)b * Co + o) * Nout + n] = val;
-    }
-    __shared__ float sh[TPB], sh2[TPB];
-    sh[tid] = (n < Nout) ? val : 0.f;
-    sh2[tid] = (n < Nout) ? val * val : 0.f;
+        for (int t = 0; t < 10; ++t) { s[t] = expf(s[t] - mx); sum += s[t]; }
+        float inv = 1.f / sum;
+#pragma unroll
+        for (int t = 0; t < 10; ++t) {
+            if (valid[t]) {
+                float zv = z[((size_t)b * 160 + t * 16 + o) * 1500 + col[t]];
+                val = fmaf(s[t] * inv, zv, val);
+            }
+        }
+        out[((size_t)b * 16 + o) * 750 + n] = val;
+    }
+    sh[tid] = (n < 750) ? val : 0.f;
+    sh2[tid] = (n < 750) ? val * val : 0.f;
     __syncthreads();
     for (int st = TPB / 2; st > 0; st >>= 1) {
         if (tid < st) { sh[tid] += sh[tid + st]; sh2[tid] += sh2[tid + st]; }
         __syncthreads();
     }
-    if (tid == 0) {
-        int chunk = b * gridDim.x + blockIdx.x;
-        part[(size_t)o * (2 * gridDim.x) + chunk] = make_float2(sh[0], sh2[0]);
-    }
+    if (tid == 0)
+        part[(size_t)o * 6 + b * 3 + bx] = make_float2(sh[0], sh2[0]);
 }
 
 __global__ void bn_avg_final_kernel(const float* __restrict__ x,
@@ -751,65 +799,47 @@
     size_t off = 0;
     auto alloc = [&](size_t n) { float* p = ws + off; off += (n + 63) & ~(size_t)63; return p; };
 
-    float* par0   = alloc(321);
     float* part0  = alloc(64 * 188 * 2);
-    float* mr0    = alloc(128);
     float* h0raw  = alloc(2 * 64 * 6000);
     float* G1     = alloc(64 * 64);
     float* Wy1    = alloc(512 * 64);
-    float* embs1  = alloc(40);
+    float* embs1  = alloc(64);
+    float* Wcat2  = alloc(192 * 128);
     float* attn1  = alloc(2 * 10 * 6000);
     float* ybuf   = alloc(2 * 512 * 6000);
     float* part1  = alloc(128 * 48 * 2);
-    float* mr1    = alloc(256);
     float* h1raw  = alloc(2 * 128 * 1500);
-    float* Wcat2  = alloc(192 * 128);
     float* qk2    = alloc(2 * 1500 * 32);
     float* z2     = alloc(2 * 160 * 1500);
-    float* attn2  = alloc(2 * 10 * 750);
     float* part2  = alloc(16 * 6 * 2);
     float* s2     = alloc(2 * 16 * 750);
 
     auto grid = [](int n) { return (n + TPB - 1) / TPB; };
 
-    prep0_kernel<<<1, TPB, 0, stream>>>(ea0, eb0, em0, qw0, kw0, vw0, par0);
     {
-        dim3 g(94, 2, 2);
-        attn_out0_kernel<<<g, TPB, 0, stream>>>(x, par0, h0raw, (float2*)part0);
-    }
-    prep_stage1_kernel<<<64, TPB, 0, stream>>>(ea1, eb1, em1, qw1, kw1, vw1,
-        G1, Wy1, embs1, (const float2*)part0, mr0);
-    {
-        dim3 g(24, 4, 2);
-        attn_v4_kernel<<<g, TPB, 0, stream>>>(G1, h0raw, mr0, g0, b0, attn1);
-    }
-    {
-        dim3 g(47, 4, 2);
-        gemm_qkbn_kernel<<<g, TPB, 0, stream>>>(Wy1, h0raw, mr0, g0, b0,
-            ybuf , ybuf, 512, 6000, 64, 0);
-    }
+        dim3 g(102, 2, 2);
+        stage0_kernel<<<g, TPB, 0, stream>>>(x,
+            qw0, kw0, vw0, ea0, eb0, em0,
+            qw1, kw1, vw1, ea1, eb1, em1,
+            qw2, kw2, vw2, ea2, eb2, em2,
+            h0raw, (float2*)part0, G1, Wy1, embs1, Wcat2);
+    }
+    stage1_dual_kernel<<<568, TPB, 0, stream>>>(G1, Wy1, h0raw,
+        (const float2*)part0, g0, b0, attn1, ybuf);
     {
         dim3 g(24, 256);
         combine1_kernel<<<g, TPB, 0, stream>>>(ybuf, attn1, embs1,
             h1raw, (float2*)part1);
     }
-    prep_wcat_kernel<<<24, TPB, 0, stream>>>(ea2, eb2, em2, qw2, kw2, vw2, Wcat2,
-        16, 2, 5, 128, (const float2*)part1, mr1, 128, 48, 12000);
     {
         dim3 g(12, 2, 2);
-        gemm_qkbn_kernel<<<g, TPB, 0, stream>>>(Wcat2, h1raw, mr1, g1, b1,
-            qk2, z2, 192, 1500, 128, 32);
+        gemm2_kernel<<<g, TPB, 0, stream>>>(Wcat2, h1raw,
+            (const float2*)part1, g1, b1, qk2, z2);
     }
     {
-        dim3 g(750 / 25, 2);
-        attn_v3_kernel<2, 5, 16, 25><<<g, TPB, 0, stream>>>(qk2, attn2,
-            2, 750, 1, 750, 0, 2);
-    }
-    {
-        dim3 g(3, 2 * 16);
-        combine_stats_kernel<2, 5><<<g, TPB, 0, stream>>>(z2, attn2, s2,
-            (float2*)part2, 16, 160, 2, 750, 1, 750, 0, 2);
-    }
-    bn_avg_final_kernel<<<grid(2 * 16 * 13), TPB, 0, stream>>>(s2, (const float2*)part2,
-        g2, b2, outp, 2, 16, 750, 13, 6);
+        dim3 g(3, 32);
+        attn_combine2_kernel<<<g, TPB, 0, stream>>>(qk2, z2, s2, (float2*)part2);
+    }
+    bn_avg_final_kernel<<<grid(2 * 16 * 13), TPB, 0, stream>>>(s2,
+        (const float2*)part2, g2, b2, outp, 2, 16, 750, 13, 6);
 }
```

Measured after the change: 275.6 us. +6.0%, slower.
